# Performance work log

Measured on AMD Instinct MI355X. Metric: run time of the kernel, lower is better.

The kernel has to match this reference:

```python
import jax, jax.numpy as jnp
import numpy as np

MI_N, DIS_N = 16384, 8192
EM = 128
E_MM, E_DD = MI_N * 32, DIS_N * 32


def _add_self_loops(edges, ew, n):
    loop = jnp.arange(n, dtype=edges.dtype)
    row = jnp.concatenate([edges[0], loop])
    col = jnp.concatenate([edges[1], loop])
    ew = jnp.concatenate([ew, jnp.ones((n,), ew.dtype)])
    return row, col, ew


def gcn_conv(x, edges, w, b, n, ew=None):
    # PyG GCNConv: symmetric gcn_norm with self-loops (fill 1.0), then
    # out[col] += norm * (x @ w)[row], plus bias.
    if ew is None:
        ew = jnp.ones((edges.shape[1],), x.dtype)
    row, col, ew = _add_self_loops(edges, ew, n)
    deg = jax.ops.segment_sum(ew, col, num_segments=n)
    dinv = jnp.where(deg > 0, jax.lax.rsqrt(deg), 0.0)
    norm = dinv[row] * ew * dinv[col]          # [E+n]
    h = x @ w                                   # [n, d]
    return jax.ops.segment_sum(h[row] * norm[:, None], col, num_segments=n) + b


def gat_conv(x, edges, w, a_src, a_dst, b, n):
    # PyG GATConv, heads=1: per-edge attention LeakyReLU(0.2) + softmax over
    # incoming edges of each target node (self-loops added).
    h = x @ w                                   # [n, d]
    row, col, _ = _add_self_loops(edges, jnp.ones((edges.shape[1],), x.dtype), n)
    e = jax.nn.leaky_relu((h @ a_src)[row] + (h @ a_dst)[col], negative_slope=0.2)
    m = jax.ops.segment_max(e, col, num_segments=n)
    ex = jnp.exp(e - m[col])
    s = jax.ops.segment_sum(ex, col, num_segments=n)
    alpha = ex / s[col]                         # [E+n]
    return jax.ops.segment_sum(h[row] * alpha[:, None], col, num_segments=n) + b


def setup_inputs() -> dict:
    key = jax.random.key(0)
    ks = jax.random.split(key, 24)
    sc = 1.0 / np.sqrt(EM)
    d = {
        'mm_x0': jax.random.normal(ks[0], (MI_N, EM), jnp.float32),
        'dd_x0': jax.random.normal(ks[1], (DIS_N, EM), jnp.float32),
        'w1_mm': jax.random.normal(ks[2], (EM, EM), jnp.float32) * sc,
        'b1_mm': jnp.zeros((EM,), jnp.float32),
        'w2_mm': jax.random.normal(ks[3], (EM, EM), jnp.float32) * sc,
        'b2_mm': jnp.zeros((EM,), jnp.float32),
        'w3_mm': jax.random.normal(ks[4], (EM, EM), jnp.float32) * sc,
        'asrc_mm': jax.random.normal(ks[5], (EM,), jnp.float32) * sc,
        'adst_mm': jax.random.normal(ks[6], (EM,), jnp.float32) * sc,
        'b3_mm': jnp.zeros((EM,), jnp.float32),
        'w1_dd': jax.random.normal(ks[7], (EM, EM), jnp.float32) * sc,
        'b1_dd': jnp.zeros((EM,), jnp.float32),
        'w2_dd': jax.random.normal(ks[8], (EM, EM), jnp.float32) * sc,
        'b2_dd': jnp.zeros((EM,), jnp.float32),
        'w3_dd': jax.random.normal(ks[9], (EM, EM), jnp.float32) * sc,
        'asrc_dd': jax.random.normal(ks[10], (EM,), jnp.float32) * sc,
        'adst_dd': jax.random.normal(ks[11], (EM,), jnp.float32) * sc,
        'b3_dd': jnp.zeros((EM,), jnp.float32),
        'mm_ew': jax.random.uniform(ks[12], (E_MM,), jnp.float32),
        'dd_ew': jax.random.uniform(ks[13], (E_DD,), jnp.float32),
        'mm_edges': jax.random.randint(ks[14], (2, E_MM), 0, MI_N, jnp.int32),
        'dd_edges': jax.random.randint(ks[15], (2, E_DD), 0, DIS_N, jnp.int32),
    }
    return d


def reference(mm_x0, dd_x0, w1_mm, b1_mm, w2_mm, b2_mm, w3_mm, asrc_mm, adst_mm,
              b3_mm, w1_dd, b1_dd, w2_dd, b2_dd, w3_dd, asrc_dd, adst_dd, b3_dd,
              mm_ew, dd_ew, mm_edges, dd_edges):
    elu = jax.nn.elu
    m1 = elu(gcn_conv(mm_x0, mm_edges, w1_mm, b1_mm, MI_N, mm_ew))
    m2 = elu(gcn_conv(m1, mm_edges, w2_mm, b2_mm, MI_N))
    m3 = elu(gat_conv(m2, mm_edges, w3_mm, asrc_mm, adst_mm, b3_mm, MI_N))
    d1 = elu(gcn_conv(dd_x0, dd_edges, w1_dd, b1_dd, DIS_N, dd_ew))
    d2 = elu(gcn_conv(d1, dd_edges, w2_dd, b2_dd, DIS_N))
    d3 = elu(gat_conv(d2, dd_edges, w3_dd, asrc_dd, adst_dd, b3_dd, DIS_N))
    mi_fea = (m1 + m2 + m3) / 3.0
    dis_fea = (d1 + d2 + d3) / 3.0
    score_raw = mi_fea @ dis_fea.T              # [MI_N, DIS_N]
    mn, mx = jnp.min(score_raw), jnp.max(score_raw)
    denom = jnp.where(mx > mn, mx - mn, jnp.asarray(1.0, score_raw.dtype))
    score_norm = jnp.where(mx > mn, (score_raw - mn) / denom,
                           jnp.zeros_like(score_raw))
    score_norm = jnp.clip(score_norm, 0.0, 1.0)
    return score_norm, mi_fea, dis_fea
```

## Files before the change

### kernel.cpp

```cpp
#include <hip/hip_runtime.h>
#include <cstdint>
#include <cstddef>

#define MI_NN 16384
#define DIS_NN 8192
#define EMB 128
#define EMM (MI_NN*32)
#define EDD (DIS_NN*32)

typedef __attribute__((ext_vector_type(8))) short short8;
typedef __attribute__((ext_vector_type(4))) float f32x4;

__device__ __forceinline__ float leakyr(float x){ return x > 0.f ? x : 0.2f*x; }
__device__ __forceinline__ float eluf(float x){ return x > 0.f ? x : expm1f(x); }

__device__ __forceinline__ unsigned bf16u(float x){
  unsigned u = __float_as_uint(x);
  return (u + 0x7FFFu + ((u >> 16) & 1u)) >> 16;
}
__device__ __forceinline__ float bfl(unsigned p){ return __uint_as_float(p << 16); }
__device__ __forceinline__ float bfh(unsigned p){ return __uint_as_float(p & 0xFFFF0000u); }

__global__ __launch_bounds__(256) void k_count2g(const int* __restrict__ c0, int* __restrict__ n0c,
                                                 int E0, int nb0,
                                                 const int* __restrict__ c1, int* __restrict__ n1c,
                                                 int E1){
  int b = blockIdx.x;
  const int* col; int* cnt; int E; int t;
  if (b < nb0){ col = c0; cnt = n0c; E = E0; t = b*256 + threadIdx.x; }
  else        { col = c1; cnt = n1c; E = E1; t = (b - nb0)*256 + threadIdx.x; }
  if (t < E) atomicAdd(&cnt[col[t]], 1);
}

__global__ __launch_bounds__(1024) void k_scan2g(const int* __restrict__ cnt0, int* __restrict__ rp0,
                                                 int n0, int E0,
                                                 const int* __restrict__ cnt1, int* __restrict__ rp1,
                                                 int n1, int E1){
  const int* cnt = blockIdx.x ? cnt1 : cnt0;
  int* rowptr    = blockIdx.x ? rp1  : rp0;
  int n          = blockIdx.x ? n1   : n0;
  int E          = blockIdx.x ? E1   : E0;
  __shared__ int lds[1024];
  int t = threadIdx.x;
  int chunk = n >> 10;
  int base = t*chunk;
  int s = 0;
  for (int i = 0; i < chunk; ++i) s += cnt[base+i];
  lds[t] = s; __syncthreads();
  for (int off = 1; off < 1024; off <<= 1){
    int v = (t >= off) ? lds[t-off] : 0;
    __syncthreads();
    lds[t] += v;
    __syncthreads();
  }
  int run = lds[t] - s;
  for (int i = 0; i < chunk; ++i){ rowptr[base+i] = run; run += cnt[base+i]; }
  if (t == 0) rowptr[n] = E;
}

__global__ __launch_bounds__(256) void k_fill2g(
    const int* __restrict__ r0a, const int* __restrict__ c0a, const float* __restrict__ w0a,
    const int* __restrict__ rp0, int* __restrict__ f0, int2* __restrict__ e0,
    int E0, int nb0,
    const int* __restrict__ r1a, const int* __restrict__ c1a, const float* __restrict__ w1a,
    const int* __restrict__ rp1, int* __restrict__ f1, int2* __restrict__ e1,
    int E1){
  int b = blockIdx.x;
  const int *row, *col; const float* ew; const int* rowptr;
  int* fill; int2* epk; int E, t;
  if (b < nb0){ row=r0a; col=c0a; ew=w0a; rowptr=rp0; fill=f0; epk=e0; E=E0; t=b*256+threadIdx.x; }
  else        { row=r1a; col=c1a; ew=w1a; rowptr=rp1; fill=f1; epk=e1; E=E1; t=(b-nb0)*256+threadIdx.x; }
  if (t < E){
    int c = col[t];
    int p = rowptr[c] + atomicAdd(&fill[c], 1);
    epk[p] = make_int2(row[t], __float_as_int(ew[t]));
  }
}

template<int FUSE>
__global__ __launch_bounds__(256) void k_gemm2g(
    const float* __restrict__ X0, const float* __restrict__ W0, ushort* __restrict__ H0, int nb0,
    const float* __restrict__ X1, const float* __restrict__ W1, ushort* __restrict__ H1,
    const float* __restrict__ as0, const float* __restrict__ ad0,
    float* __restrict__ es0, float* __restrict__ ed0,
    const float* __restrict__ as1, const float* __restrict__ ad1,
    float* __restrict__ es1, float* __restrict__ ed1){
  int b = blockIdx.x;
  const float *X, *W, *asr, *ads; ushort* H; float *es, *ed; int rb;
  if (b < nb0){ X=X0; W=W0; H=H0; asr=as0; ads=ad0; es=es0; ed=ed0; rb = b; }
  else        { X=X1; W=W1; H=H1; asr=as1; ads=ad1; es=es1; ed=ed1; rb = b - nb0; }
  __shared__ float wl[EMB*EMB];
  int t = threadIdx.x;
  {
    const float4* W4 = (const float4*)W;
    float4* L4 = (float4*)wl;
    #pragma unroll
    for (int i = 0; i < 16; ++i) L4[t + 256*i] = W4[t + 256*i];
  }
  __syncthreads();
  int jg = t & 31;
  int rg = t >> 5;
  int r0 = rb*32 + rg*4;
  f32x4 acc0 = {0,0,0,0}, acc1 = {0,0,0,0}, acc2 = {0,0,0,0}, acc3 = {0,0,0,0};
  const float4* X4 = (const float4*)X;
  for (int k4 = 0; k4 < 32; ++k4){
    float4 x0 = X4[(size_t)(r0+0)*32 + k4];
    float4 x1 = X4[(size_t)(r0+1)*32 + k4];
    float4 x2 = X4[(size_t)(r0+2)*32 + k4];
    float4 x3 = X4[(size_t)(r0+3)*32 + k4];
#define GSTEP(c0,c1,c2,c3,kq) { f32x4 w4 = *(const f32x4*)&wl[(kq)*EMB + jg*4]; \
      acc0 += (c0)*w4; acc1 += (c1)*w4; acc2 += (c2)*w4; acc3 += (c3)*w4; }
    GSTEP(x0.x, x1.x, x2.x, x3.x, k4*4+0)
    GSTEP(x0.y, x1.y, x2.y, x3.y, k4*4+1)
    GSTEP(x0.z, x1.z, x2.z, x3.z, k4*4+2)
    GSTEP(x0.w, x1.w, x2.w, x3.w, k4*4+3)
#undef GSTEP
  }
#define PACK2(o, a) { o.x = bf16u(a[0]) | (bf16u(a[1])<<16); o.y = bf16u(a[2]) | (bf16u(a[3])<<16); }
  uint2 o0, o1, o2, o3;
  PACK2(o0, acc0) PACK2(o1, acc1) PACK2(o2, acc2) PACK2(o3, acc3)
#undef PACK2
  ushort* out = H + (size_t)r0*EMB + jg*4;
  *(uint2*)(out)         = o0;
  *(uint2*)(out + EMB)   = o1;
  *(uint2*)(out + 2*EMB) = o2;
  *(uint2*)(out + 3*EMB) = o3;

  if (FUSE){
    f32x4 s4 = *(const f32x4*)&asr[jg*4];
    f32x4 d4 = *(const f32x4*)&ads[jg*4];
    float ps0 = acc0[0]*s4[0] + acc0[1]*s4[1] + acc0[2]*s4[2] + acc0[3]*s4[3];
    float ps1 = acc1[0]*s4[0] + acc1[1]*s4[1] + acc1[2]*s4[2] + acc1[3]*s4[3];
    float ps2 = acc2[0]*s4[0] + acc2[1]*s4[1] + acc2[2]*s4[2] + acc2[3]*s4[3];
    float ps3 = acc3[0]*s4[0] + acc3[1]*s4[1] + acc3[2]*s4[2] + acc3[3]*s4[3];
    float pd0 = acc0[0]*d4[0] + acc0[1]*d4[1] + acc0[2]*d4[2] + acc0[3]*d4[3];
    float pd1 = acc1[0]*d4[0] + acc1[1]*d4[1] + acc1[2]*d4[2] + acc1[3]*d4[3];
    float pd2 = acc2[0]*d4[0] + acc2[1]*d4[1] + acc2[2]*d4[2] + acc2[3]*d4[3];
    float pd3 = acc3[0]*d4[0] + acc3[1]*d4[1] + acc3[2]*d4[2] + acc3[3]*d4[3];
    #pragma unroll
    for (int off = 16; off; off >>= 1){
      ps0 += __shfl_xor(ps0, off); ps1 += __shfl_xor(ps1, off);
      ps2 += __shfl_xor(ps2, off); ps3 += __shfl_xor(ps3, off);
      pd0 += __shfl_xor(pd0, off); pd1 += __shfl_xor(pd1, off);
      pd2 += __shfl_xor(pd2, off); pd3 += __shfl_xor(pd3, off);
    }
    if (jg == 0){
      es[r0+0] = ps0; es[r0+1] = ps1; es[r0+2] = ps2; es[r0+3] = ps3;
      ed[r0+0] = pd0; ed[r0+1] = pd1; ed[r0+2] = pd2; ed[r0+3] = pd3;
    }
  }
}

__global__ __launch_bounds__(256) void k_deg2g(
    const int* __restrict__ rp0, const int2* __restrict__ ep0,
    float* __restrict__ d10, float* __restrict__ d20, int n0, int nb0,
    const int* __restrict__ rp1, const int2* __restrict__ ep1,
    float* __restrict__ d11, float* __restrict__ d21, int n1){
  int b = blockIdx.x;
  const int* rowptr; const int2* epk; float *d1, *d2; int n, wid;
  int lane = threadIdx.x & 63;
  if (b < nb0){ rowptr=rp0; epk=ep0; d1=d10; d2=d20; n=n0; wid = (b*256 + threadIdx.x) >> 6; }
  else        { rowptr=rp1; epk=ep1; d1=d11; d2=d21; n=n1; wid = ((b-nb0)*256 + threadIdx.x) >> 6; }
  if (wid >= n) return;
  int beg = rowptr[wid], end = rowptr[wid+1];
  float s = 0.f;
  for (int i = beg + lane; i < end; i += 64) s += __int_as_float(epk[i].y);
  #pragma unroll
  for (int off = 32; off; off >>= 1) s += __shfl_xor(s, off);
  if (lane == 0){
    d1[wid] = rsqrtf(1.0f + s);
    d2[wid] = rsqrtf(1.0f + (float)(end - beg));
  }
}

__global__ __launch_bounds__(256) void k_agg2g(
    const ushort* __restrict__ H0, const float* __restrict__ di0, const int* __restrict__ rp0,
    const int2* __restrict__ ep0, const float* __restrict__ bi0,
    float* __restrict__ xn0, float* __restrict__ fe0, int n0, int nb0,
    const ushort* __restrict__ H1, const float* __restrict__ di1, const int* __restrict__ rp1,
    const int2* __restrict__ ep1, const float* __restrict__ bi1,
    float* __restrict__ xn1, float* __restrict__ fe1, int n1,
    int useew, int femode){
  int b = blockIdx.x;
  const ushort* H; const float* dinv; const int* rowptr; const int2* epk;
  const float* bias; float* xnext; float* fea; int n, wid;
  int lane = threadIdx.x & 63;
  if (b < nb0){ H=H0; dinv=di0; rowptr=rp0; epk=ep0; bias=bi0; xnext=xn0; fea=fe0; n=n0;
                wid = (b*256 + threadIdx.x) >> 6; }
  else        { H=H1; dinv=di1; rowptr=rp1; epk=ep1; bias=bi1; xnext=xn1; fea=fe1; n=n1;
                wid = ((b-nb0)*256 + threadIdx.x) >> 6; }
  if (wid >= n) return;
  int v = wid;
  float dv = dinv[v];
  unsigned hb = *(const unsigned*)(H + (size_t)v*EMB + lane*2);
  float ax = dv*bfl(hb), ay = dv*bfh(hb);
  int beg = rowptr[v], end = rowptr[v+1];
  int i = beg;
  int e4 = beg + ((end - beg) & ~3);
  for (; i < e4; i += 4){
    int2 e0 = epk[i], e1 = epk[i+1], e2 = epk[i+2], e3 = epk[i+3];
    float n0v = dinv[e0.x], n1v = dinv[e1.x], n2v = dinv[e2.x], n3v = dinv[e3.x];
    if (useew){ n0v *= __int_as_float(e0.y); n1v *= __int_as_float(e1.y);
                n2v *= __int_as_float(e2.y); n3v *= __int_as_float(e3.y); }
    unsigned h0 = *(const unsigned*)(H + (size_t)e0.x*EMB + lane*2);
    unsigned h1 = *(const unsigned*)(H + (size_t)e1.x*EMB + lane*2);
    unsigned h2 = *(const unsigned*)(H + (size_t)e2.x*EMB + lane*2);
    unsigned h3 = *(const unsigned*)(H + (size_t)e3.x*EMB + lane*2);
    ax += n0v*bfl(h0) + n1v*bfl(h1) + n2v*bfl(h2) + n3v*bfl(h3);
    ay += n0v*bfh(h0) + n1v*bfh(h1) + n2v*bfh(h2) + n3v*bfh(h3);
  }
  for (; i < end; ++i){
    int2 e = epk[i];
    float nm = dinv[e.x];
    if (useew) nm *= __int_as_float(e.y);
    unsigned hr = *(const unsigned*)(H + (size_t)e.x*EMB + lane*2);
    ax += nm*bfl(hr); ay += nm*bfh(hr);
  }
  float2 b2 = ((const float2*)bias)[lane];
  float ox = eluf(dv*ax + b2.x), oy = eluf(dv*ay + b2.y);
  ((float2*)xnext)[(size_t)v*64 + lane] = make_float2(ox, oy);
  float2* F2 = (float2*)fea;
  if (femode == 0){
    F2[(size_t)v*64 + lane] = make_float2(ox, oy);
  } else {
    float2 f = F2[(size_t)v*64 + lane];
    F2[(size_t)v*64 + lane] = make_float2(f.x + ox, f.y + oy);
  }
}

__global__ __launch_bounds__(256) void k_gat2g(
    const ushort* __restrict__ H0, const float* __restrict__ es0, const float* __restrict__ ed0,
    const int* __restrict__ rp0, const int2* __restrict__ ep0, const float* __restrict__ bi0,
    float* __restrict__ fe0, unsigned* __restrict__ sh0, int n0, int nb0,
    const ushort* __restrict__ H1, const float* __restrict__ es1, const float* __restrict__ ed1,
    const int* __restrict__ rp1, const int2* __restrict__ ep1, const float* __restrict__ bi1,
    float* __restrict__ fe1, unsigned* __restrict__ sh1, int n1){
  int b = blockIdx.x;
  const ushort* H; const float *es, *ed; const int* rowptr; const int2* epk; const float* bias;
  float* fea; unsigned* shadow; int n, wid;
  int lane = threadIdx.x & 63;
  if (b < nb0){ H=H0; es=es0; ed=ed0; rowptr=rp0; epk=ep0; bias=bi0; fea=fe0; shadow=sh0; n=n0;
                wid = (b*256 + threadIdx.x) >> 6; }
  else        { H=H1; es=es1; ed=ed1; rowptr=rp1; epk=ep1; bias=bi1; fea=fe1; shadow=sh1; n=n1;
                wid = ((b-nb0)*256 + threadIdx.x) >> 6; }
  if (wid >= n) return;
  int v = wid;
  float edv = ed[v];
  float self_e = leakyr(es[v] + edv);
  int beg = rowptr[v], end = rowptr[v+1];
  float m = -3.4e38f, s = 0.f;
  for (int i = beg + lane; i < end; i += 64){
    float e = leakyr(es[epk[i].x] + edv);
    if (e > m){ s = s*expf(m - e) + 1.0f; m = e; }
    else s += expf(e - m);
  }
  #pragma unroll
  for (int off = 32; off; off >>= 1){
    float m2 = __shfl_xor(m, off), s2 = __shfl_xor(s, off);
    float mn_ = fmaxf(m, m2);
    s = s*expf(m - mn_) + s2*expf(m2 - mn_);
    m = mn_;
  }
  {
    float mn_ = fmaxf(m, self_e);
    s = s*expf(m - mn_) + expf(self_e - mn_);
    m = mn_;
  }
  float inv_s = 1.0f / s;
  unsigned hb = *(const unsigned*)(H + (size_t)v*EMB + lane*2);
  float a0 = expf(self_e - m)*inv_s;
  float ax = a0*bfl(hb), ay = a0*bfh(hb);
  int i = beg;
  int e4 = beg + ((end - beg) & ~3);
  for (; i < e4; i += 4){
    int r0 = epk[i].x, r1 = epk[i+1].x, r2 = epk[i+2].x, r3 = epk[i+3].x;
    float a_0 = expf(leakyr(es[r0] + edv) - m)*inv_s;
    float a_1 = expf(leakyr(es[r1] + edv) - m)*inv_s;
    float a_2 = expf(leakyr(es[r2] + edv) - m)*inv_s;
    float a_3 = expf(leakyr(es[r3] + edv) - m)*inv_s;
    unsigned h0 = *(const unsigned*)(H + (size_t)r0*EMB + lane*2);
    unsigned h1 = *(const unsigned*)(H + (size_t)r1*EMB + lane*2);
    unsigned h2 = *(const unsigned*)(H + (size_t)r2*EMB + lane*2);
    unsigned h3 = *(const unsigned*)(H + (size_t)r3*EMB + lane*2);
    ax += a_0*bfl(h0) + a_1*bfl(h1) + a_2*bfl(h2) + a_3*bfl(h3);
    ay += a_0*bfh(h0) + a_1*bfh(h1) + a_2*bfh(h2) + a_3*bfh(h3);
  }
  for (; i < end; ++i){
    int r = epk[i].x;
    float a = expf(leakyr(es[r] + edv) - m)*inv_s;
    unsigned hr = *(const unsigned*)(H + (size_t)r*EMB + lane*2);
    ax += a*bfl(hr); ay += a*bfh(hr);
  }
  float2 b2 = ((const float2*)bias)[lane];
  float ox = eluf(ax + b2.x), oy = eluf(ay + b2.y);
  float2* F2 = (float2*)fea;
  float2 f = F2[(size_t)v*64 + lane];
  float fx = (f.x + ox)/3.0f, fy = (f.y + oy)/3.0f;
  F2[(size_t)v*64 + lane] = make_float2(fx, fy);
  shadow[(size_t)v*64 + lane] = bf16u(fx) | (bf16u(fy) << 16);
}

__device__ __forceinline__ void stage128(const uint8_t* G, uint8_t* L, int w, int lane){
  #pragma unroll
  for (int c = 0; c < 8; ++c){
    int linear = w*8192 + c*1024 + lane*16;
    int row = linear >> 8, col = linear & 255;
    const void* src = G + row*256 + (col ^ ((row & 7) << 4));
    __builtin_amdgcn_global_load_lds(
        (const __attribute__((address_space(1))) void*)src,
        (__attribute__((address_space(3))) void*)(L + w*8192 + c*1024),
        16, 0, 0);
  }
}

#define NT 16
template<int STORE>
__global__ __launch_bounds__(256) void k_score5(const ushort* __restrict__ Abf,
                                                const ushort* __restrict__ Bbf,
                                                float* __restrict__ S,
                                                float* __restrict__ mmpart){
  __shared__ __align__(16) uint8_t L0[32768];
  __shared__ __align__(16) uint8_t L1[32768];
  __shared__ float red[16];
  const int t = threadIdx.x;
  const int lane = t & 63;
  const int w = t >> 6;
  const int wr = w >> 1, wc = w & 1;
  const int lr = lane & 15, lk = lane >> 4;
  const int i0b = blockIdx.y * 128;
  const int jbase = blockIdx.x * NT;

  stage128((const uint8_t*)(Abf + (size_t)i0b*EMB), L0, w, lane);
  stage128((const uint8_t*)(Bbf + (size_t)jbase*128*EMB), L1, w, lane);
  __syncthreads();

  short8 af[4][4];
  #pragma unroll
  for (int at = 0; at < 4; ++at){
    int ra = wr*64 + at*16 + lr;
    #pragma unroll
    for (int k0 = 0; k0 < 4; ++k0){
      int kb = k0*64 + lk*16;
      af[at][k0] = *(const short8*)&L0[ra*256 + (kb ^ ((ra & 7) << 4))];
    }
  }
  __syncthreads();
  stage128((const uint8_t*)(Bbf + (size_t)(jbase+1)*128*EMB), L0, w, lane);

  float mn = 0.f, sc = 0.f;
  if (STORE){
    mn = mmpart[0];
    float mx = mmpart[1];
    sc = (mx > mn) ? 1.0f/(mx - mn) : 0.0f;
  }
  float lmin = 3.4e38f, lmax = -3.4e38f;

  for (int jt = 0; jt < NT; ++jt){
    uint8_t* curB = (jt & 1) ? L0 : L1;
    f32x4 acc[4][4];
    #pragma unroll
    for (int a = 0; a < 4; ++a)
      #pragma unroll
      for (int b = 0; b < 4; ++b) acc[a][b] = (f32x4){0.f,0.f,0.f,0.f};

    #pragma unroll
    for (int k0 = 0; k0 < 4; ++k0){
      int kb = k0*64 + lk*16;
      short8 bfr[4];
      #pragma unroll
      for (int ct = 0; ct < 4; ++ct){
        int rb = wc*64 + ct*16 + lr;
        bfr[ct] = *(const short8*)&curB[rb*256 + (kb ^ ((rb & 7) << 4))];
      }
      #pragma unroll
      for (int at = 0; at < 4; ++at)
        #pragma unroll
        for (int ct = 0; ct < 4; ++ct)
          acc[at][ct] = __builtin_amdgcn_mfma_f32_16x16x32_bf16(af[at][k0], bfr[ct], acc[at][ct], 0, 0, 0);
    }

    int j0 = (jbase + jt)*128;
    if (STORE){
      #pragma unroll
      for (int at = 0; at < 4; ++at){
        #pragma unroll
        for (int ct = 0; ct < 4; ++ct){
          int colj = j0 + wc*64 + ct*16 + lr;
          int row0 = i0b + wr*64 + at*16 + lk*4;
          #pragma unroll
          for (int q = 0; q < 4; ++q){
            float vv = fminf(fmaxf((acc[at][ct][q] - mn)*sc, 0.f), 1.f);
            S[(size_t)(row0+q)*DIS_NN + colj] = vv;
          }
        }
      }
    } else {
      #pragma unroll
      for (int at = 0; at < 4; ++at)
        #pragma unroll
        for (int ct = 0; ct < 4; ++ct)
          #pragma unroll
          for (int q = 0; q < 4; ++q){
            float vv = acc[at][ct][q];
            lmin = fminf(lmin, vv); lmax = fmaxf(lmax, vv);
          }
    }
    __syncthreads();
    if (jt + 2 < NT)
      stage128((const uint8_t*)(Bbf + (size_t)(jbase+jt+2)*128*EMB), curB, w, lane);
  }

  if (!STORE){
    #pragma unroll
    for (int off = 32; off; off >>= 1){
      lmin = fminf(lmin, __shfl_xor(lmin, off));
      lmax = fmaxf(lmax, __shfl_xor(lmax, off));
    }
    if (lane == 0){ red[w*2] = lmin; red[w*2+1] = lmax; }
    __syncthreads();
    if (t == 0){
      float a = fminf(fminf(red[0], red[2]), fminf(red[4], red[6]));
      float b = fmaxf(fmaxf(red[1], red[3]), fmaxf(red[5], red[7]));
      int bid = blockIdx.y * 4 + blockIdx.x;
      mmpart[2 + bid*2]     = a;
      mmpart[2 + bid*2 + 1] = b;
    }
  }
}

__global__ __launch_bounds__(512) void k_mmred(float* __restrict__ mm){
  __shared__ float2 red[8];
  int t = threadIdx.x;
  float mn = mm[2 + t*2];
  float mx = mm[2 + t*2 + 1];
  #pragma unroll
  for (int off = 32; off; off >>= 1){
    mn = fminf(mn, __shfl_xor(mn, off));
    mx = fmaxf(mx, __shfl_xor(mx, off));
  }
  if ((t & 63) == 0) red[t >> 6] = make_float2(mn, mx);
  __syncthreads();
  if (t == 0){
    float a = red[0].x, b = red[0].y;
    #pragma unroll
    for (int i = 1; i < 8; ++i){ a = fminf(a, red[i].x); b = fmaxf(b, red[i].y); }
    mm[0] = a; mm[1] = b;
  }
}

extern "C" void kernel_launch(void* const* d_in, const int* in_sizes, int n_in,
                              void* d_out, int out_size, void* d_ws, size_t ws_size,
                              hipStream_t stream){
  (void)in_sizes; (void)n_in; (void)out_size; (void)ws_size;
  const float* mm_x0  = (const float*)d_in[0];
  const float* dd_x0  = (const float*)d_in[1];
  const float* w1_mm  = (const float*)d_in[2];
  const float* b1_mm  = (const float*)d_in[3];
  const float* w2_mm  = (const float*)d_in[4];
  const float* b2_mm  = (const float*)d_in[5];
  const float* w3_mm  = (const float*)d_in[6];
  const float* asrc_mm= (const float*)d_in[7];
  const float* adst_mm= (const float*)d_in[8];
  const float* b3_mm  = (const float*)d_in[9];
  const float* w1_dd  = (const float*)d_in[10];
  const float* b1_dd  = (const float*)d_in[11];
  const float* w2_dd  = (const float*)d_in[12];
  const float* b2_dd  = (const float*)d_in[13];
  const float* w3_dd  = (const float*)d_in[14];
  const float* asrc_dd= (const float*)d_in[15];
  const float* adst_dd= (const float*)d_in[16];
  const float* b3_dd  = (const float*)d_in[17];
  const float* mm_ew  = (const float*)d_in[18];
  const float* dd_ew  = (const float*)d_in[19];
  const int* mm_edges = (const int*)d_in[20];
  const int* dd_edges = (const int*)d_in[21];

  float* S = (float*)d_out;
  float* p = S;
  float* A0m = p;  p += (size_t)MI_NN*EMB;
  float* A1m = p;  p += (size_t)MI_NN*EMB;
  float* A0d = p;  p += (size_t)DIS_NN*EMB;
  float* A1d = p;  p += (size_t)DIS_NN*EMB;
  ushort* Hbm = (ushort*)p; p += (size_t)MI_NN*EMB/2;
  ushort* Hbd = (ushort*)p; p += (size_t)DIS_NN*EMB/2;
  float* DEG1m = p; p += MI_NN;
  float* DEG2m = p; p += MI_NN;
  float* ESm   = p; p += MI_NN;
  float* EDm   = p; p += MI_NN;
  float* DEG1d = p; p += DIS_NN;
  float* DEG2d = p; p += DIS_NN;
  float* ESd   = p; p += DIS_NN;
  float* EDd   = p; p += DIS_NN;
  int* CNTm  = (int*)p; p += MI_NN;
  int* CNTd  = (int*)p; p += DIS_NN;
  int* FILLm = (int*)p; p += MI_NN;
  int* FILLd = (int*)p; p += DIS_NN;
  int* RPm   = (int*)p; p += MI_NN + 64;
  int* RPd   = (int*)p; p += DIS_NN + 64;
  int2* EPKm = (int2*)p; p += (size_t)EMM*2;
  int2* EPKd = (int2*)p; p += (size_t)EDD*2;
  float* FEA_MI  = S + (size_t)MI_NN * DIS_NN;
  float* FEA_DIS = FEA_MI + (size_t)MI_NN*EMB;

  float* MM = (float*)d_ws;
  ushort* Abf = (ushort*)((char*)d_ws + 16384);
  ushort* Bbf = Abf + (size_t)MI_NN * EMB;

  const int* erow_m = mm_edges;
  const int* ecol_m = mm_edges + EMM;
  const int* erow_d = dd_edges;
  const int* ecol_d = dd_edges + EDD;

  hipMemsetAsync(CNTm, 0, (size_t)2*(MI_NN + DIS_NN)*sizeof(int), stream);
  k_count2g<<<EMM/256 + EDD/256, 256, 0, stream>>>(ecol_m, CNTm, EMM, EMM/256,
                                                   ecol_d, CNTd, EDD);
  k_scan2g<<<2, 1024, 0, stream>>>(CNTm, RPm, MI_NN, EMM, CNTd, RPd, DIS_NN, EDD);
  k_fill2g<<<EMM/256 + EDD/256, 256, 0, stream>>>(erow_m, ecol_m, mm_ew, RPm, FILLm, EPKm,
                                                  EMM, EMM/256,
                                                  erow_d, ecol_d, dd_ew, RPd, FILLd, EPKd,
                                                  EDD);
  const int GB = MI_NN/32 + DIS_NN/32;
  const int AB = MI_NN/4 + DIS_NN/4;
  k_gemm2g<0><<<GB, 256, 0, stream>>>(mm_x0, w1_mm, Hbm, MI_NN/32, dd_x0, w1_dd, Hbd,
                                      nullptr, nullptr, nullptr, nullptr,
                                      nullptr, nullptr, nullptr, nullptr);
  k_deg2g<<<AB, 256, 0, stream>>>(RPm, EPKm, DEG1m, DEG2m, MI_NN, MI_NN/4,
                                  RPd, EPKd, DEG1d, DEG2d, DIS_NN);
  k_agg2g<<<AB, 256, 0, stream>>>(Hbm, DEG1m, RPm, EPKm, b1_mm, A0m, FEA_MI, MI_NN, MI_NN/4,
                                  Hbd, DEG1d, RPd, EPKd, b1_dd, A0d, FEA_DIS, DIS_NN, 1, 0);
  k_gemm2g<0><<<GB, 256, 0, stream>>>(A0m, w2_mm, Hbm, MI_NN/32, A0d, w2_dd, Hbd,
                                      nullptr, nullptr, nullptr, nullptr,
                                      nullptr, nullptr, nullptr, nullptr);
  k_agg2g<<<AB, 256, 0, stream>>>(Hbm, DEG2m, RPm, EPKm, b2_mm, A1m, FEA_MI, MI_NN, MI_NN/4,
                                  Hbd, DEG2d, RPd, EPKd, b2_dd, A1d, FEA_DIS, DIS_NN, 0, 1);
  k_gemm2g<1><<<GB, 256, 0, stream>>>(A1m, w3_mm, Hbm, MI_NN/32, A1d, w3_dd, Hbd,
                                      asrc_mm, adst_mm, ESm, EDm,
                                      asrc_dd, adst_dd, ESd, EDd);
  k_gat2g<<<AB, 256, 0, stream>>>(Hbm, ESm, EDm, RPm, EPKm, b3_mm, FEA_MI, (unsigned*)Abf, MI_NN, MI_NN/4,
                                  Hbd, ESd, EDd, RPd, EPKd, b3_dd, FEA_DIS, (unsigned*)Bbf, DIS_NN);
  k_score5<0><<<dim3(DIS_NN/(128*NT), MI_NN/128), 256, 0, stream>>>(Abf, Bbf, nullptr, MM);
  k_mmred<<<1, 512, 0, stream>>>(MM);
  k_score5<1><<<dim3(DIS_NN/(128*NT), MI_NN/128), 256, 0, stream>>>(Abf, Bbf, S, MM);
}
```

Before: 434.2 us.

## Split wavefront into half-waves for 8-byte gathers; fold min/max reduce into score kernel

The GCN and GAT aggregation kernels now split each 64-lane wave into two halves. Each half processes alternate edges, each lane gathers four bf16 features with an 8-byte load, and the halves are combined with a cross-half shuffle before a vectorised float4 epilogue. The intent is fewer, wider gather instructions and more independent edge loads in flight. Separately, the standalone min/max reduction kernel is removed: the last block of the first score pass, detected with an atomic counter reset in the count kernel, does the final reduction. This saves one launch but adds a threadfence and atomic per block.

```diff
diff --git a/kernel.cpp b/kernel.cpp
--- a/kernel.cpp
+++ b/kernel.cpp
@@ -24,7 +24,8 @@
 __global__ __launch_bounds__(256) void k_count2g(const int* __restrict__ c0, int* __restrict__ n0c,
                                                  int E0, int nb0,
                                                  const int* __restrict__ c1, int* __restrict__ n1c,
-                                                 int E1){
+                                                 int E1, unsigned* __restrict__ ctr){
+  if (blockIdx.x == 0 && threadIdx.x == 0) ctr[0] = 0u;
   int b = blockIdx.x;
   const int* col; int* cnt; int E; int t;
   if (b < nb0){ col = c0; cnt = n0c; E = E0; t = b*256 + threadIdx.x; }
@@ -191,40 +192,48 @@
                 wid = ((b-nb0)*256 + threadIdx.x) >> 6; }
   if (wid >= n) return;
   int v = wid;
+  int half = lane >> 5;
+  int hl   = lane & 31;
   float dv = dinv[v];
-  unsigned hb = *(const unsigned*)(H + (size_t)v*EMB + lane*2);
-  float ax = dv*bfl(hb), ay = dv*bfh(hb);
+  uint2 hv = *(const uint2*)(H + (size_t)v*EMB + hl*4);
+  float a0, a1, a2, a3;
+  if (half == 0){
+    a0 = dv*bfl(hv.x); a1 = dv*bfh(hv.x); a2 = dv*bfl(hv.y); a3 = dv*bfh(hv.y);
+  } else { a0 = a1 = a2 = a3 = 0.f; }
   int beg = rowptr[v], end = rowptr[v+1];
-  int i = beg;
-  int e4 = beg + ((end - beg) & ~3);
-  for (; i < e4; i += 4){
-    int2 e0 = epk[i], e1 = epk[i+1], e2 = epk[i+2], e3 = epk[i+3];
-    float n0v = dinv[e0.x], n1v = dinv[e1.x], n2v = dinv[e2.x], n3v = dinv[e3.x];
-    if (useew){ n0v *= __int_as_float(e0.y); n1v *= __int_as_float(e1.y);
-                n2v *= __int_as_float(e2.y); n3v *= __int_as_float(e3.y); }
-    unsigned h0 = *(const unsigned*)(H + (size_t)e0.x*EMB + lane*2);
-    unsigned h1 = *(const unsigned*)(H + (size_t)e1.x*EMB + lane*2);
-    unsigned h2 = *(const unsigned*)(H + (size_t)e2.x*EMB + lane*2);
-    unsigned h3 = *(const unsigned*)(H + (size_t)e3.x*EMB + lane*2);
-    ax += n0v*bfl(h0) + n1v*bfl(h1) + n2v*bfl(h2) + n3v*bfl(h3);
-    ay += n0v*bfh(h0) + n1v*bfh(h1) + n2v*bfh(h2) + n3v*bfh(h3);
-  }
-  for (; i < end; ++i){
+  int i = beg + half;
+  for (; i + 2 < end; i += 4){
+    int2 eA = epk[i], eB = epk[i+2];
+    float nA = dinv[eA.x], nB = dinv[eB.x];
+    if (useew){ nA *= __int_as_float(eA.y); nB *= __int_as_float(eB.y); }
+    uint2 hA = *(const uint2*)(H + (size_t)eA.x*EMB + hl*4);
+    uint2 hB = *(const uint2*)(H + (size_t)eB.x*EMB + hl*4);
+    a0 += nA*bfl(hA.x) + nB*bfl(hB.x);
+    a1 += nA*bfh(hA.x) + nB*bfh(hB.x);
+    a2 += nA*bfl(hA.y) + nB*bfl(hB.y);
+    a3 += nA*bfh(hA.y) + nB*bfh(hB.y);
+  }
+  if (i < end){
     int2 e = epk[i];
     float nm = dinv[e.x];
     if (useew) nm *= __int_as_float(e.y);
-    unsigned hr = *(const unsigned*)(H + (size_t)e.x*EMB + lane*2);
-    ax += nm*bfl(hr); ay += nm*bfh(hr);
-  }
-  float2 b2 = ((const float2*)bias)[lane];
-  float ox = eluf(dv*ax + b2.x), oy = eluf(dv*ay + b2.y);
-  ((float2*)xnext)[(size_t)v*64 + lane] = make_float2(ox, oy);
-  float2* F2 = (float2*)fea;
-  if (femode == 0){
-    F2[(size_t)v*64 + lane] = make_float2(ox, oy);
-  } else {
-    float2 f = F2[(size_t)v*64 + lane];
-    F2[(size_t)v*64 + lane] = make_float2(f.x + ox, f.y + oy);
+    uint2 h = *(const uint2*)(H + (size_t)e.x*EMB + hl*4);
+    a0 += nm*bfl(h.x); a1 += nm*bfh(h.x); a2 += nm*bfl(h.y); a3 += nm*bfh(h.y);
+  }
+  a0 += __shfl_xor(a0, 32); a1 += __shfl_xor(a1, 32);
+  a2 += __shfl_xor(a2, 32); a3 += __shfl_xor(a3, 32);
+  if (half == 0){
+    float4 b4 = *(const float4*)(bias + hl*4);
+    float o0 = eluf(dv*a0 + b4.x), o1 = eluf(dv*a1 + b4.y);
+    float o2 = eluf(dv*a2 + b4.z), o3 = eluf(dv*a3 + b4.w);
+    *(float4*)(xnext + (size_t)v*EMB + hl*4) = make_float4(o0, o1, o2, o3);
+    float* fp = fea + (size_t)v*EMB + hl*4;
+    if (femode == 0){
+      *(float4*)fp = make_float4(o0, o1, o2, o3);
+    } else {
+      float4 f = *(float4*)fp;
+      *(float4*)fp = make_float4(f.x + o0, f.y + o1, f.z + o2, f.w + o3);
+    }
   }
 }
 
@@ -267,37 +276,48 @@
     m = mn_;
   }
   float inv_s = 1.0f / s;
-  unsigned hb = *(const unsigned*)(H + (size_t)v*EMB + lane*2);
-  float a0 = expf(self_e - m)*inv_s;
-  float ax = a0*bfl(hb), ay = a0*bfh(hb);
-  int i = beg;
-  int e4 = beg + ((end - beg) & ~3);
-  for (; i < e4; i += 4){
-    int r0 = epk[i].x, r1 = epk[i+1].x, r2 = epk[i+2].x, r3 = epk[i+3].x;
-    float a_0 = expf(leakyr(es[r0] + edv) - m)*inv_s;
-    float a_1 = expf(leakyr(es[r1] + edv) - m)*inv_s;
-    float a_2 = expf(leakyr(es[r2] + edv) - m)*inv_s;
-    float a_3 = expf(leakyr(es[r3] + edv) - m)*inv_s;
-    unsigned h0 = *(const unsigned*)(H + (size_t)r0*EMB + lane*2);
-    unsigned h1 = *(const unsigned*)(H + (size_t)r1*EMB + lane*2);
-    unsigned h2 = *(const unsigned*)(H + (size_t)r2*EMB + lane*2);
-    unsigned h3 = *(const unsigned*)(H + (size_t)r3*EMB + lane*2);
-    ax += a_0*bfl(h0) + a_1*bfl(h1) + a_2*bfl(h2) + a_3*bfl(h3);
-    ay += a_0*bfh(h0) + a_1*bfh(h1) + a_2*bfh(h2) + a_3*bfh(h3);
-  }
-  for (; i < end; ++i){
+  int half = lane >> 5;
+  int hl   = lane & 31;
+  uint2 hv = *(const uint2*)(H + (size_t)v*EMB + hl*4);
+  float aw = expf(self_e - m)*inv_s;
+  float a0, a1, a2, a3;
+  if (half == 0){
+    a0 = aw*bfl(hv.x); a1 = aw*bfh(hv.x); a2 = aw*bfl(hv.y); a3 = aw*bfh(hv.y);
+  } else { a0 = a1 = a2 = a3 = 0.f; }
+  int i = beg + half;
+  for (; i + 2 < end; i += 4){
+    int rA = epk[i].x, rB = epk[i+2].x;
+    float aA = expf(leakyr(es[rA] + edv) - m)*inv_s;
+    float aB = expf(leakyr(es[rB] + edv) - m)*inv_s;
+    uint2 hA = *(const uint2*)(H + (size_t)rA*EMB + hl*4);
+    uint2 hB = *(const uint2*)(H + (size_t)rB*EMB + hl*4);
+    a0 += aA*bfl(hA.x) + aB*bfl(hB.x);
+    a1 += aA*bfh(hA.x) + aB*bfh(hB.x);
+    a2 += aA*bfl(hA.y) + aB*bfl(hB.y);
+    a3 += aA*bfh(hA.y) + aB*bfh(hB.y);
+  }
+  if (i < end){
     int r = epk[i].x;
     float a = expf(leakyr(es[r] + edv) - m)*inv_s;
-    unsigned hr = *(const unsigned*)(H + (size_t)r*EMB + lane*2);
-    ax += a*bfl(hr); ay += a*bfh(hr);
-  }
-  float2 b2 = ((const float2*)bias)[lane];
-  float ox = eluf(ax + b2.x), oy = eluf(ay + b2.y);
-  float2* F2 = (float2*)fea;
-  float2 f = F2[(size_t)v*64 + lane];
-  float fx = (f.x + ox)/3.0f, fy = (f.y + oy)/3.0f;
-  F2[(size_t)v*64 + lane] = make_float2(fx, fy);
-  shadow[(size_t)v*64 + lane] = bf16u(fx) | (bf16u(fy) << 16);
+    uint2 h = *(const uint2*)(H + (size_t)r*EMB + hl*4);
+    a0 += a*bfl(h.x); a1 += a*bfh(h.x); a2 += a*bfl(h.y); a3 += a*bfh(h.y);
+  }
+  a0 += __shfl_xor(a0, 32); a1 += __shfl_xor(a1, 32);
+  a2 += __shfl_xor(a2, 32); a3 += __shfl_xor(a3, 32);
+  if (half == 0){
+    float4 b4 = *(const float4*)(bias + hl*4);
+    float o0 = eluf(a0 + b4.x), o1 = eluf(a1 + b4.y);
+    float o2 = eluf(a2 + b4.z), o3 = eluf(a3 + b4.w);
+    float* fp = fea + (size_t)v*EMB + hl*4;
+    float4 f = *(float4*)fp;
+    float f0 = (f.x + o0)/3.0f, f1 = (f.y + o1)/3.0f;
+    float f2 = (f.z + o2)/3.0f, f3 = (f.w + o3)/3.0f;
+    *(float4*)fp = make_float4(f0, f1, f2, f3);
+    uint2 sh;
+    sh.x = bf16u(f0) | (bf16u(f1) << 16);
+    sh.y = bf16u(f2) | (bf16u(f3) << 16);
+    *(uint2*)(shadow + (size_t)v*64 + hl*2) = sh;
+  }
 }
 
 __device__ __forceinline__ void stage128(const uint8_t* G, uint8_t* L, int w, int lane){
@@ -322,6 +342,7 @@
   __shared__ __align__(16) uint8_t L0[32768];
   __shared__ __align__(16) uint8_t L1[32768];
   __shared__ float red[16];
+  __shared__ unsigned sdone;
   const int t = threadIdx.x;
   const int lane = t & 63;
   const int w = t >> 6;
@@ -418,33 +439,34 @@
     }
     if (lane == 0){ red[w*2] = lmin; red[w*2+1] = lmax; }
     __syncthreads();
+    unsigned* ctr = (unsigned*)(mmpart + 1088);
     if (t == 0){
       float a = fminf(fminf(red[0], red[2]), fminf(red[4], red[6]));
       float b = fmaxf(fmaxf(red[1], red[3]), fmaxf(red[5], red[7]));
       int bid = blockIdx.y * 4 + blockIdx.x;
       mmpart[2 + bid*2]     = a;
       mmpart[2 + bid*2 + 1] = b;
-    }
-  }
-}
-
-__global__ __launch_bounds__(512) void k_mmred(float* __restrict__ mm){
-  __shared__ float2 red[8];
-  int t = threadIdx.x;
-  float mn = mm[2 + t*2];
-  float mx = mm[2 + t*2 + 1];
-  #pragma unroll
-  for (int off = 32; off; off >>= 1){
-    mn = fminf(mn, __shfl_xor(mn, off));
-    mx = fmaxf(mx, __shfl_xor(mx, off));
-  }
-  if ((t & 63) == 0) red[t >> 6] = make_float2(mn, mx);
-  __syncthreads();
-  if (t == 0){
-    float a = red[0].x, b = red[0].y;
-    #pragma unroll
-    for (int i = 1; i < 8; ++i){ a = fminf(a, red[i].x); b = fmaxf(b, red[i].y); }
-    mm[0] = a; mm[1] = b;
+      __threadfence();
+      sdone = atomicAdd(ctr, 1u);
+    }
+    __syncthreads();
+    if (sdone == 511u){
+      __threadfence();
+      float mnv = fminf(mmpart[2 + 2*t], mmpart[2 + 2*(t+256)]);
+      float mxv = fmaxf(mmpart[3 + 2*t], mmpart[3 + 2*(t+256)]);
+      #pragma unroll
+      for (int off = 32; off; off >>= 1){
+        mnv = fminf(mnv, __shfl_xor(mnv, off));
+        mxv = fmaxf(mxv, __shfl_xor(mxv, off));
+      }
+      if (lane == 0){ red[w*2] = mnv; red[w*2+1] = mxv; }
+      __syncthreads();
+      if (t == 0){
+        float a = fminf(fminf(red[0], red[2]), fminf(red[4], red[6]));
+        float b = fmaxf(fmaxf(red[1], red[3]), fmaxf(red[5], red[7]));
+        mmpart[0] = a; mmpart[1] = b;
+      }
+    }
   }
 }
 
@@ -513,7 +535,8 @@
 
   hipMemsetAsync(CNTm, 0, (size_t)2*(MI_NN + DIS_NN)*sizeof(int), stream);
   k_count2g<<<EMM/256 + EDD/256, 256, 0, stream>>>(ecol_m, CNTm, EMM, EMM/256,
-                                                   ecol_d, CNTd, EDD);
+                                                   ecol_d, CNTd, EDD,
+                                                   (unsigned*)(MM + 1088));
   k_scan2g<<<2, 1024, 0, stream>>>(CNTm, RPm, MI_NN, EMM, CNTd, RPd, DIS_NN, EDD);
   k_fill2g<<<EMM/256 + EDD/256, 256, 0, stream>>>(erow_m, ecol_m, mm_ew, RPm, FILLm, EPKm,
                                                   EMM, EMM/256,
@@ -539,6 +562,5 @@
   k_gat2g<<<AB, 256, 0, stream>>>(Hbm, ESm, EDm, RPm, EPKm, b3_mm, FEA_MI, (unsigned*)Abf, MI_NN, MI_NN/4,
                                   Hbd, ESd, EDd, RPd, EPKd, b3_dd, FEA_DIS, (unsigned*)Bbf, DIS_NN);
   k_score5<0><<<dim3(DIS_NN/(128*NT), MI_NN/128), 256, 0, stream>>>(Abf, Bbf, nullptr, MM);
-  k_mmred<<<1, 512, 0, stream>>>(MM);
   k_score5<1><<<dim3(DIS_NN/(128*NT), MI_NN/128), 256, 0, stream>>>(Abf, Bbf, S, MM);
 }
```

Result: no change. 437.3 us (+0.7%).
